# Kernel tuning notes

Hardware: AMD Instinct MI355X
Metric: run time of the kernel (lower is better)

## Reference

```python
import jax, jax.numpy as jnp
import numpy as np

ROWS = 1_000_000
COLS = 1_000_000
NNZ_PER_ROW = 32
NNZ = ROWS * NNZ_PER_ROW


def setup_inputs() -> dict:
    key = jax.random.key(0)
    k1, k2 = jax.random.split(key)
    x = jax.random.normal(k1, (COLS,), dtype=jnp.float32)
    values = jax.random.normal(k2, (NNZ,), dtype=jnp.float32)
    k3 = jax.random.fold_in(key, 3)
    col_indices = jax.random.randint(k3, (NNZ,), 0, COLS, dtype=jnp.int32)
    # Valid CSR row pointers: uniform NNZ_PER_ROW nonzeros per row.
    row_ptrs = (jnp.arange(ROWS + 1, dtype=jnp.int32) * NNZ_PER_ROW)
    return {"x": x, "values": values, "col_indices": col_indices, "row_ptrs": row_ptrs}


def reference(x, values, col_indices, row_ptrs):
    """CSR SpMV: y[i] = sum_{j in [row_ptrs[i], row_ptrs[i+1])} values[j] * x[col_indices[j]].
    Vectorized as a gather + segmented sum (same math as the manual per-element loop)."""
    nnz = values.shape[0]
    rows = row_ptrs.shape[0] - 1
    # Row id of each nonzero: the row whose [start, end) interval contains j.
    row_ids = jnp.searchsorted(row_ptrs, jnp.arange(nnz, dtype=row_ptrs.dtype), side="right") - 1
    prod = values * x[col_indices]          # [nnz]
    y = jax.ops.segment_sum(prod, row_ids, num_segments=rows)  # [rows]
    return y
```

## Files before the change

kernel.cpp:

```cpp
#include <hip/hip_runtime.h>


__global__ __launch_bounds__(256) void spmv_csr32_kernel(
    const float* __restrict__ x,
    const float* __restrict__ vals,
    const int*   __restrict__ cols,
    const int*   __restrict__ rp,
    float*       __restrict__ y,
    int rows)
{
    const int tid   = blockIdx.x * blockDim.x + threadIdx.x;
    const int row   = tid >> 3;
    const int lane8 = tid & 7;
    if (row >= rows) return;

    const int start = rp[row];
    const int end   = rp[row + 1];

    float sum = 0.0f;
    if (end - start == 32) {
        const int j = start + lane8 * 4;
        const float4 v = *reinterpret_cast<const float4*>(vals + j);
        const int4   c = *reinterpret_cast<const int4*>(cols + j);
        sum = v.x * x[c.x] + v.y * x[c.y] + v.z * x[c.z] + v.w * x[c.w];
    } else {
        for (int k = start + lane8; k < end; k += 8)
            sum += vals[k] * x[cols[k]];
    }

    sum += __shfl_xor(sum, 1);
    sum += __shfl_xor(sum, 2);
    sum += __shfl_xor(sum, 4);

    if (lane8 == 0) y[row] = sum;
}

extern "C" void kernel_launch(void* const* d_in, const int* in_sizes, int n_in,
                              void* d_out, int out_size, void* d_ws, size_t ws_size,
                              hipStream_t stream)
{
    const float* x    = (const float*)d_in[0];
    const float* vals = (const float*)d_in[1];
    const int*   cols = (const int*)d_in[2];
    const int*   rp   = (const int*)d_in[3];
    float*       y    = (float*)d_out;

    const int rows = out_size;
    const int threads = rows * 8;
    const int block = 256;
    const int grid = (threads + block - 1) / block;

    spmv_csr32_kernel<<<grid, block, 0, stream>>>(x, vals, cols, rp, y, rows);
}
```

Before: 183.0 us.

## Use two threads per row with nontemporal vector loads and more gathers in flight

```diff
diff --git a/kernel.cpp b/kernel.cpp
--- a/kernel.cpp
+++ b/kernel.cpp
@@ -1,5 +1,8 @@
 #include <hip/hip_runtime.h>
 
+
+typedef float f32x4 __attribute__((ext_vector_type(4)));
+typedef int   i32x4 __attribute__((ext_vector_type(4)));
 
 __global__ __launch_bounds__(256) void spmv_csr32_kernel(
     const float* __restrict__ x,
@@ -9,30 +12,47 @@
     float*       __restrict__ y,
     int rows)
 {
-    const int tid   = blockIdx.x * blockDim.x + threadIdx.x;
-    const int row   = tid >> 3;
-    const int lane8 = tid & 7;
+    const int tid = blockIdx.x * blockDim.x + threadIdx.x;
+    const int row = tid >> 1;
+    const int l2  = tid & 1;
     if (row >= rows) return;
 
-    const int start = rp[row];
-    const int end   = rp[row + 1];
+    const int mine  = __builtin_nontemporal_load(rp + row + l2);
+    const int other = __shfl_xor(mine, 1);
+    const int start = l2 ? other : mine;
+    const int end   = l2 ? mine  : other;
 
     float sum = 0.0f;
     if (end - start == 32) {
-        const int j = start + lane8 * 4;
-        const float4 v = *reinterpret_cast<const float4*>(vals + j);
-        const int4   c = *reinterpret_cast<const int4*>(cols + j);
-        sum = v.x * x[c.x] + v.y * x[c.y] + v.z * x[c.z] + v.w * x[c.w];
+        const int j = start + l2 * 4;
+
+        const i32x4 c0 = __builtin_nontemporal_load(reinterpret_cast<const i32x4*>(cols + j));
+        const i32x4 c1 = __builtin_nontemporal_load(reinterpret_cast<const i32x4*>(cols + j + 8));
+        const i32x4 c2 = __builtin_nontemporal_load(reinterpret_cast<const i32x4*>(cols + j + 16));
+        const i32x4 c3 = __builtin_nontemporal_load(reinterpret_cast<const i32x4*>(cols + j + 24));
+
+        const float x00 = x[c0[0]], x01 = x[c0[1]], x02 = x[c0[2]], x03 = x[c0[3]];
+        const float x10 = x[c1[0]], x11 = x[c1[1]], x12 = x[c1[2]], x13 = x[c1[3]];
+        const float x20 = x[c2[0]], x21 = x[c2[1]], x22 = x[c2[2]], x23 = x[c2[3]];
+        const float x30 = x[c3[0]], x31 = x[c3[1]], x32 = x[c3[2]], x33 = x[c3[3]];
+
+        const f32x4 v0 = __builtin_nontemporal_load(reinterpret_cast<const f32x4*>(vals + j));
+        const f32x4 v1 = __builtin_nontemporal_load(reinterpret_cast<const f32x4*>(vals + j + 8));
+        const f32x4 v2 = __builtin_nontemporal_load(reinterpret_cast<const f32x4*>(vals + j + 16));
+        const f32x4 v3 = __builtin_nontemporal_load(reinterpret_cast<const f32x4*>(vals + j + 24));
+
+        sum = v0[0]*x00 + v0[1]*x01 + v0[2]*x02 + v0[3]*x03
+            + v1[0]*x10 + v1[1]*x11 + v1[2]*x12 + v1[3]*x13
+            + v2[0]*x20 + v2[1]*x21 + v2[2]*x22 + v2[3]*x23
+            + v3[0]*x30 + v3[1]*x31 + v3[2]*x32 + v3[3]*x33;
     } else {
-        for (int k = start + lane8; k < end; k += 8)
+        for (int k = start + l2; k < end; k += 2)
             sum += vals[k] * x[cols[k]];
     }
 
     sum += __shfl_xor(sum, 1);
-    sum += __shfl_xor(sum, 2);
-    sum += __shfl_xor(sum, 4);
 
-    if (lane8 == 0) y[row] = sum;
+    if (l2 == 0) y[row] = sum;
 }
 
 extern "C" void kernel_launch(void* const* d_in, const int* in_sizes, int n_in,
@@ -46,7 +66,7 @@
     float*       y    = (float*)d_out;
 
     const int rows = out_size;
-    const int threads = rows * 8;
+    const int threads = rows * 2;
     const int block = 256;
     const int grid = (threads + block - 1) / block;
 
```

Measured after the change: 204.2 us. +11.6%, slower.
